# Performance work log

Measured on AMD Instinct MI355X. Metric: run time of the kernel, lower is better.

The kernel has to match this reference:

```python
import jax, jax.numpy as jnp
import numpy as np


def _lerp_idx(in_size, out_size):
    # align_corners=True mapping: src = dst * (in-1)/(out-1)
    pos = jnp.arange(out_size, dtype=jnp.float32) * ((in_size - 1) / (out_size - 1))
    i0 = jnp.clip(jnp.floor(pos).astype(jnp.int32), 0, in_size - 2)
    w = pos - i0.astype(jnp.float32)
    return i0, i0 + 1, w


def _upsample_bilinear_ac(x, scale):
    # x: [B,C,H,W] -> [B,C,H*scale,W*scale], separable bilinear, align_corners=True
    B, C, H, W = x.shape
    Ho, Wo = H * scale, W * scale
    i0, i1, wy = _lerp_idx(H, Ho)
    j0, j1, wx = _lerp_idx(W, Wo)
    wy = wy[None, None, :, None]
    rows = x[:, :, i0, :] * (1.0 - wy) + x[:, :, i1, :] * wy  # [B,C,Ho,W]
    wx = wx[None, None, None, :]
    return rows[:, :, :, j0] * (1.0 - wx) + rows[:, :, :, j1] * wx  # [B,C,Ho,Wo]


def setup_inputs() -> dict:
    key = jax.random.key(0)
    k1, k2, k3 = jax.random.split(key, 3)
    x = jax.random.normal(k1, (4, 64, 96, 320), dtype=jnp.float32)
    weight = jax.random.normal(k2, (1, 64, 1, 1), dtype=jnp.float32) * 0.125
    bias = jax.random.normal(k3, (1,), dtype=jnp.float32) * 0.1
    return {"x": x, "weight": weight, "bias": bias}


def reference(x, weight, bias):
    SCALE = 4
    up = _upsample_bilinear_ac(x, SCALE)                     # [B,C,Ho,Wo]
    w2 = weight[:, :, 0, 0]                                   # [1,C]
    y = jnp.einsum('bchw,oc->bohw', up, w2) + bias[None, :, None, None]
    return jax.nn.relu(y)
```

## Files before the change

### kernel.cpp

```cpp
#include <hip/hip_runtime.h>


constexpr int C = 64, H = 96, W = 320, HW = H * W;
constexpr int Ho = 384, Wo = 1280;
constexpr int HW4 = HW / 4;

__global__ __launch_bounds__(256)
void reduce_c_kernel(const float* __restrict__ x,
                     const float* __restrict__ wgt,
                     float* __restrict__ z)
{
    __shared__ float ws[C];
    const int tid = threadIdx.x;
    if (tid < C) ws[tid] = wgt[tid];
    __syncthreads();

    const int gt = blockIdx.x * 256 + tid;
    const int q  = gt >> 2;
    const int lc = gt & 3;
    const int b  = q / HW4;
    const int s  = (q - b * HW4) * 4;

    const float* p = x + (size_t)b * C * HW + s;
    float4 acc = make_float4(0.f, 0.f, 0.f, 0.f);
    #pragma unroll
    for (int k = 0; k < 16; ++k) {
        const int ch = lc * 16 + k;
        const float4 v = *(const float4*)(p + (size_t)ch * HW);
        const float wv = ws[ch];
        acc.x += v.x * wv; acc.y += v.y * wv;
        acc.z += v.z * wv; acc.w += v.w * wv;
    }
    acc.x += __shfl_xor(acc.x, 1); acc.y += __shfl_xor(acc.y, 1);
    acc.z += __shfl_xor(acc.z, 1); acc.w += __shfl_xor(acc.w, 1);
    acc.x += __shfl_xor(acc.x, 2); acc.y += __shfl_xor(acc.y, 2);
    acc.z += __shfl_xor(acc.z, 2); acc.w += __shfl_xor(acc.w, 2);

    if (lc == 0) ((float4*)z)[q] = acc;
}

__global__ __launch_bounds__(256)
void upsample_kernel(const float* __restrict__ z,
                     const float* __restrict__ bias,
                     float* __restrict__ out)
{
    const float RH = 95.0f / 383.0f;
    const float RW = 319.0f / 1279.0f;

    const int gt = blockIdx.x * 256 + threadIdx.x;
    const int o  = gt * 4;
    const int b  = o / (Ho * Wo);
    const int r  = o - b * (Ho * Wo);
    const int oh = r / Wo;
    const int ow = r - oh * Wo;

    const float ph = (float)oh * RH;
    const int   i0 = min((int)ph, H - 2);
    const float wy = ph - (float)i0;

    const float* z0 = z + ((size_t)b * H + i0) * W;
    const float* z1 = z0 + W;
    const float bv = bias[0];

    float vals[4];
    #pragma unroll
    for (int j = 0; j < 4; ++j) {
        const float pw = (float)(ow + j) * RW;
        const int   j0 = min((int)pw, W - 2);
        const float wx = pw - (float)j0;
        const float top = z0[j0] * (1.f - wx) + z0[j0 + 1] * wx;
        const float bot = z1[j0] * (1.f - wx) + z1[j0 + 1] * wx;
        const float v   = top * (1.f - wy) + bot * wy + bv;
        vals[j] = fmaxf(v, 0.f);
    }
    ((float4*)out)[gt] = make_float4(vals[0], vals[1], vals[2], vals[3]);
}

extern "C" void kernel_launch(void* const* d_in, const int* in_sizes, int n_in,
                              void* d_out, int out_size, void* d_ws, size_t ws_size,
                              hipStream_t stream) {
    const float* x    = (const float*)d_in[0];
    const float* wgt  = (const float*)d_in[1];
    const float* bias = (const float*)d_in[2];
    float* out = (float*)d_out;
    float* z   = (float*)d_ws;

    reduce_c_kernel<<<dim3((4 * HW4 * 4) / 256), 256, 0, stream>>>(x, wgt, z);
    upsample_kernel<<<dim3((4 * Ho * Wo / 4) / 256), 256, 0, stream>>>(z, bias, out);
}
```

Baseline: 80.97 us.

## Fuse channel reduction and bilinear upsample into one tiled kernel

Merges the two kernels into one. Each workgroup computes its output tile's channel-reduced input patch into shared memory, then upsamples from LDS. This removes the global intermediate and one launch, and block IDs are swizzled to spread work. The cost is recomputing halo rows and columns across tiles, plus a reduction phase that uses only 240 of 256 threads with fewer loads in flight.

```diff
diff --git a/kernel.cpp b/kernel.cpp
--- a/kernel.cpp
+++ b/kernel.cpp
@@ -3,88 +3,103 @@
 
 constexpr int C = 64, H = 96, W = 320, HW = H * W;
 constexpr int Ho = 384, Wo = 1280;
-constexpr int HW4 = HW / 4;
+constexpr int TOH = 16, TOW = 128;
+constexpr int NTR = Ho / TOH;
+constexpr int NTC = Wo / TOW;
+constexpr int NWG = 4 * NTR * NTC;
+constexpr int ZR = 6, ZC = 40;
 
 __global__ __launch_bounds__(256)
-void reduce_c_kernel(const float* __restrict__ x,
-                     const float* __restrict__ wgt,
-                     float* __restrict__ z)
+void fused_kernel(const float* __restrict__ x,
+                  const float* __restrict__ wgt,
+                  const float* __restrict__ bias,
+                  float* __restrict__ out)
 {
+    constexpr float RH = 95.0f / 383.0f;
+    constexpr float RW = 319.0f / 1279.0f;
+
     __shared__ float ws[C];
+    __shared__ float zt[ZR][ZC];
+
+    int bid = blockIdx.x;
+    bid = (bid & 7) * (NWG / 8) + (bid >> 3);
+
+    const int tc = bid % NTC;
+    const int t2 = bid / NTC;
+    const int tr = t2 % NTR;
+    const int b  = t2 / NTR;
+
     const int tid = threadIdx.x;
     if (tid < C) ws[tid] = wgt[tid];
     __syncthreads();
 
-    const int gt = blockIdx.x * 256 + tid;
-    const int q  = gt >> 2;
-    const int lc = gt & 3;
-    const int b  = q / HW4;
-    const int s  = (q - b * HW4) * 4;
+    const int oh0  = tr * TOH;
+    const int ow0  = tc * TOW;
+    const int r_lo = min((int)((float)oh0 * RH), H - 2);
+    const int j_lo = min((int)((float)ow0 * RW), W - 2);
+    const int jb   = j_lo & ~3;
 
-    const float* p = x + (size_t)b * C * HW + s;
-    float4 acc = make_float4(0.f, 0.f, 0.f, 0.f);
+    {
+        const int g  = tid >> 2;
+        const int lc = tid & 3;
+        if (g < ZR * (ZC / 4)) {
+            const int r  = g / (ZC / 4);
+            const int jq = g - r * (ZC / 4);
+            const int rr = min(r_lo + r, H - 1);
+            const int cj = min(jb + 4 * jq, W - 4);
+            const float* p = x + (size_t)b * C * HW + (size_t)rr * W + cj;
+            float4 acc = make_float4(0.f, 0.f, 0.f, 0.f);
+            #pragma unroll
+            for (int k = 0; k < 16; ++k) {
+                const int ch = lc * 16 + k;
+                const float4 v = *(const float4*)(p + (size_t)ch * HW);
+                const float wv = ws[ch];
+                acc.x += v.x * wv; acc.y += v.y * wv;
+                acc.z += v.z * wv; acc.w += v.w * wv;
+            }
+            acc.x += __shfl_xor(acc.x, 1); acc.y += __shfl_xor(acc.y, 1);
+            acc.z += __shfl_xor(acc.z, 1); acc.w += __shfl_xor(acc.w, 1);
+            acc.x += __shfl_xor(acc.x, 2); acc.y += __shfl_xor(acc.y, 2);
+            acc.z += __shfl_xor(acc.z, 2); acc.w += __shfl_xor(acc.w, 2);
+            if (lc == 0) *(float4*)&zt[r][4 * jq] = acc;
+        }
+    }
+    __syncthreads();
+
+    const float bv   = bias[0];
+    const int   fq   = tid & 31;
+    const int   rb   = tid >> 5;
     #pragma unroll
-    for (int k = 0; k < 16; ++k) {
-        const int ch = lc * 16 + k;
-        const float4 v = *(const float4*)(p + (size_t)ch * HW);
-        const float wv = ws[ch];
-        acc.x += v.x * wv; acc.y += v.y * wv;
-        acc.z += v.z * wv; acc.w += v.w * wv;
+    for (int u = 0; u < 2; ++u) {
+        const int   row = rb + 8 * u;
+        const int   oh  = oh0 + row;
+        const float phh = (float)oh * RH;
+        const int   i0  = min((int)phh, H - 2);
+        const float wy  = phh - (float)i0;
+        const float* za = zt[i0 - r_lo];
+        const float* zb = zt[i0 - r_lo + 1];
+        float vals[4];
+        #pragma unroll
+        for (int j = 0; j < 4; ++j) {
+            const int   ow = ow0 + 4 * fq + j;
+            const float pw = (float)ow * RW;
+            const int   j0 = min((int)pw, W - 2);
+            const float wx = pw - (float)j0;
+            const int   L  = j0 - jb;
+            const float top = za[L] * (1.f - wx) + za[L + 1] * wx;
+            const float bot = zb[L] * (1.f - wx) + zb[L + 1] * wx;
+            const float v   = top * (1.f - wy) + bot * wy + bv;
+            vals[j] = fmaxf(v, 0.f);
+        }
+        ((float4*)(out + ((size_t)b * Ho + oh) * Wo + ow0))[fq]
+            = make_float4(vals[0], vals[1], vals[2], vals[3]);
     }
-    acc.x += __shfl_xor(acc.x, 1); acc.y += __shfl_xor(acc.y, 1);
-    acc.z += __shfl_xor(acc.z, 1); acc.w += __shfl_xor(acc.w, 1);
-    acc.x += __shfl_xor(acc.x, 2); acc.y += __shfl_xor(acc.y, 2);
-    acc.z += __shfl_xor(acc.z, 2); acc.w += __shfl_xor(acc.w, 2);
-
-    if (lc == 0) ((float4*)z)[q] = acc;
-}
-
-__global__ __launch_bounds__(256)
-void upsample_kernel(const float* __restrict__ z,
-                     const float* __restrict__ bias,
-                     float* __restrict__ out)
-{
-    const float RH = 95.0f / 383.0f;
-    const float RW = 319.0f / 1279.0f;
-
-    const int gt = blockIdx.x * 256 + threadIdx.x;
-    const int o  = gt * 4;
-    const int b  = o / (Ho * Wo);
-    const int r  = o - b * (Ho * Wo);
-    const int oh = r / Wo;
-    const int ow = r - oh * Wo;
-
-    const float ph = (float)oh * RH;
-    const int   i0 = min((int)ph, H - 2);
-    const float wy = ph - (float)i0;
-
-    const float* z0 = z + ((size_t)b * H + i0) * W;
-    const float* z1 = z0 + W;
-    const float bv = bias[0];
-
-    float vals[4];
-    #pragma unroll
-    for (int j = 0; j < 4; ++j) {
-        const float pw = (float)(ow + j) * RW;
-        const int   j0 = min((int)pw, W - 2);
-        const float wx = pw - (float)j0;
-        const float top = z0[j0] * (1.f - wx) + z0[j0 + 1] * wx;
-        const float bot = z1[j0] * (1.f - wx) + z1[j0 + 1] * wx;
-        const float v   = top * (1.f - wy) + bot * wy + bv;
-        vals[j] = fmaxf(v, 0.f);
-    }
-    ((float4*)out)[gt] = make_float4(vals[0], vals[1], vals[2], vals[3]);
 }
 
 extern "C" void kernel_launch(void* const* d_in, const int* in_sizes, int n_in,
                               void* d_out, int out_size, void* d_ws, size_t ws_size,
                               hipStream_t stream) {
-    const float* x    = (const float*)d_in[0];
-    const float* wgt  = (const float*)d_in[1];
-    const float* bias = (const float*)d_in[2];
-    float* out = (float*)d_out;
-    float* z   = (float*)d_ws;
-
-    reduce_c_kernel<<<dim3((4 * HW4 * 4) / 256), 256, 0, stream>>>(x, wgt, z);
-    upsample_kernel<<<dim3((4 * Ho * Wo / 4) / 256), 256, 0, stream>>>(z, bias, out);
+    fused_kernel<<<dim3(NWG), 256, 0, stream>>>(
+        (const float*)d_in[0], (const float*)d_in[1],
+        (const float*)d_in[2], (float*)d_out);
 }
```

Result: no change. 79.45 us (-1.9%).
